# Kernel tuning notes

Hardware: AMD Instinct MI355X
Metric: run time of the kernel (lower is better)

The kernel has to match this reference:

```python
import jax, jax.numpy as jnp
import numpy as np

B, T, C, P = 16, 8, 64, 2048
TEMP = 1.0  # init kwarg T


def setup_inputs() -> dict:
    key = jax.random.key(0)
    ks = jax.random.split(key, 16)
    shape = (B, T, C, P)
    x = jax.random.normal(ks[0], shape, dtype=jnp.float32)
    attn = jax.random.uniform(ks[1], shape, dtype=jnp.float32)
    noise = jax.random.normal(ks[2], shape, dtype=jnp.float32)
    total = B * T * C * P
    n_noisy = int(total * 0.1)  # int(0.1 * numel), as in torch code
    idx = jax.random.permutation(ks[3], total)[:n_noisy]
    mask = jnp.zeros((total,), dtype=bool).at[idx].set(True).reshape(shape)
    perms = {}
    kidx = 4
    for i in (1, 2, 3):
        for name, dim in (("pB", B), ("pT", T), ("pC", C), ("pP", P)):
            perms[f"{name}{i}"] = jax.random.permutation(ks[kidx], dim).astype(jnp.int32)
            kidx += 1
    return dict(x=x, attn=attn, noise=noise, mask=mask, **perms)


def _permute4(x, pB, pT, pC, pP):
    # equivalent to the meshgrid/flatten gather in the torch code:
    # independent permutation along each of the 4 axes
    return x[jnp.ix_(pB, pT, pC, pP)]


def reference(x, attn, noise, mask,
              pB1, pT1, pC1, pP1,
              pB2, pT2, pC2, pP2,
              pB3, pT3, pC3, pP3):
    x_pos = jnp.where(mask, x + noise, x)
    x_neg1 = _permute4(x, pB1, pT1, pC1, pP1)
    x_neg2 = _permute4(x, pB2, pT2, pC2, pP2)
    x_neg3 = _permute4(x, pB3, pT3, pC3, pP3)

    loss_pos = jnp.mean(attn * (x - x_pos) ** 2)
    loss_neg1 = jnp.mean(attn * (x - x_neg1) ** 2)
    loss_neg2 = jnp.mean(attn * (x - x_neg2) ** 2)
    loss_neg3 = jnp.mean(attn * (x - x_neg3) ** 2)

    loss = -jnp.log(jnp.exp(loss_pos / TEMP) /
                    (jnp.exp(loss_neg1 / TEMP) + jnp.exp(loss_neg2 / TEMP) + jnp.exp(loss_neg3 / TEMP)))
    return loss
```

## Files before the change

kernel.cpp:

```cpp
#include <hip/hip_runtime.h>
#include <math.h>

#define BB 16
#define TT 8
#define CC 64
#define PP 2048
#define NROWS (BB * TT * CC)
#define TOTAL_INV (1.0f / 16777216.0f)

typedef __attribute__((address_space(1))) const void* as1_cvoid;
typedef __attribute__((address_space(3))) void* as3_void;

__device__ __forceinline__ void stage16(const float* g, float* l) {
    __builtin_amdgcn_global_load_lds((as1_cvoid)g, (as3_void)l, 16, 0, 0);
}

__global__ __launch_bounds__(256) void mask_classify_kernel(
    const unsigned char* __restrict__ mask, int* __restrict__ flag)
{
    __shared__ int sc1, sc3f;
    if (threadIdx.x == 0) { sc1 = 0; sc3f = 0; }
    __syncthreads();
    int c1 = 0, c3f = 0;
    const uint4* m4 = (const uint4*)mask;
    for (int i = threadIdx.x; i < 1024; i += 256) {
        const uint4 v = m4[i];
        const unsigned int w[4] = {v.x, v.y, v.z, v.w};
        #pragma unroll
        for (int j = 0; j < 4; ++j) {
            #pragma unroll
            for (int bt = 0; bt < 4; ++bt) {
                const unsigned int byte = (w[j] >> (8 * bt)) & 0xffu;
                c1  += (byte == 0x01u);
                c3f += (byte == 0x3fu);
            }
        }
    }
    atomicAdd(&sc1, c1);
    atomicAdd(&sc3f, c3f);
    __syncthreads();
    if (threadIdx.x == 0) {
        int f;
        if      (sc1  > 1000) f = 0;
        else if (sc3f >  600) f = 1;
        else if (sc3f >  200) f = 2;
        else if (sc1  >  200) f = 3;
        else                  f = 0;
        *flag = f;
    }
}

template <int MODE>
__device__ __forceinline__ void mask_load(const unsigned char* __restrict__ mask,
                                          size_t idx, float mf[4])
{
    if (MODE == 0) {
        const unsigned int mv = *(const unsigned int*)(mask + idx);
        #pragma unroll
        for (int k = 0; k < 4; ++k) mf[k] = ((mv >> (8 * k)) & 0xffu) ? 1.0f : 0.0f;
    } else if (MODE == 1) {
        const ushort4 mv = *(const ushort4*)((const unsigned short*)mask + idx);
        mf[0] = mv.x ? 1.0f : 0.0f; mf[1] = mv.y ? 1.0f : 0.0f;
        mf[2] = mv.z ? 1.0f : 0.0f; mf[3] = mv.w ? 1.0f : 0.0f;
    } else if (MODE == 2) {
        const float4 mv = *(const float4*)((const float*)mask + idx);
        mf[0] = mv.x != 0.f ? 1.0f : 0.0f; mf[1] = mv.y != 0.f ? 1.0f : 0.0f;
        mf[2] = mv.z != 0.f ? 1.0f : 0.0f; mf[3] = mv.w != 0.f ? 1.0f : 0.0f;
    } else {
        const int4 mv = *(const int4*)((const int*)mask + idx);
        mf[0] = mv.x ? 1.0f : 0.0f; mf[1] = mv.y ? 1.0f : 0.0f;
        mf[2] = mv.z ? 1.0f : 0.0f; mf[3] = mv.w ? 1.0f : 0.0f;
    }
}

template <int MODE>
__device__ __forceinline__ void row_body(
    const float* __restrict__ x, const float* __restrict__ attn,
    const float* __restrict__ noise, const unsigned char* __restrict__ mask,
    const int* __restrict__ pP1, const int* __restrict__ pP2,
    const int* __restrict__ pP3,
    const float* __restrict__ lds0, const float* __restrict__ lds1,
    const float* __restrict__ lds2,
    size_t rowbase, int tid, float& s0, float& s1, float& s2, float& s3)
{
    const int p0 = tid << 2;
    const int p1 = 1024 + (tid << 2);

    const float4 xv0 = *(const float4*)(x + rowbase + p0);
    const float4 xv1 = *(const float4*)(x + rowbase + p1);
    const float4 av0 = *(const float4*)(attn + rowbase + p0);
    const float4 av1 = *(const float4*)(attn + rowbase + p1);
    const float4 nv0 = *(const float4*)(noise + rowbase + p0);
    const float4 nv1 = *(const float4*)(noise + rowbase + p1);
    const int4 q10 = *(const int4*)(pP1 + p0);
    const int4 q11 = *(const int4*)(pP1 + p1);
    const int4 q20 = *(const int4*)(pP2 + p0);
    const int4 q21 = *(const int4*)(pP2 + p1);
    const int4 q30 = *(const int4*)(pP3 + p0);
    const int4 q31 = *(const int4*)(pP3 + p1);
    float mf0[4], mf1[4];
    mask_load<MODE>(mask, rowbase + p0, mf0);
    mask_load<MODE>(mask, rowbase + p1, mf1);

    const float xs0[4] = {xv0.x, xv0.y, xv0.z, xv0.w};
    const float xs1[4] = {xv1.x, xv1.y, xv1.z, xv1.w};
    const float as0[4] = {av0.x, av0.y, av0.z, av0.w};
    const float as1v[4] = {av1.x, av1.y, av1.z, av1.w};
    const float ns0[4] = {nv0.x, nv0.y, nv0.z, nv0.w};
    const float ns1[4] = {nv1.x, nv1.y, nv1.z, nv1.w};
    const int q1s0[4] = {q10.x, q10.y, q10.z, q10.w};
    const int q1s1[4] = {q11.x, q11.y, q11.z, q11.w};
    const int q2s0[4] = {q20.x, q20.y, q20.z, q20.w};
    const int q2s1[4] = {q21.x, q21.y, q21.z, q21.w};
    const int q3s0[4] = {q30.x, q30.y, q30.z, q30.w};
    const int q3s1[4] = {q31.x, q31.y, q31.z, q31.w};

    #pragma unroll
    for (int k = 0; k < 4; ++k) {
        const float d0a = ns0[k] * mf0[k];
        s0 += as0[k] * d0a * d0a;
        const float d0b = ns1[k] * mf1[k];
        s0 += as1v[k] * d0b * d0b;
    }

    __syncthreads();

    #pragma unroll
    for (int k = 0; k < 4; ++k) {
        const float d1a = xs0[k] - lds0[q1s0[k]];
        s1 += as0[k] * d1a * d1a;
        const float d2a = xs0[k] - lds1[q2s0[k]];
        s2 += as0[k] * d2a * d2a;
        const float d3a = xs0[k] - lds2[q3s0[k]];
        s3 += as0[k] * d3a * d3a;
        const float d1b = xs1[k] - lds0[q1s1[k]];
        s1 += as1v[k] * d1b * d1b;
        const float d2b = xs1[k] - lds1[q2s1[k]];
        s2 += as1v[k] * d2b * d2b;
        const float d3b = xs1[k] - lds2[q3s1[k]];
        s3 += as1v[k] * d3b * d3b;
    }
}

__global__ __launch_bounds__(256) void attn_loss_row_kernel(
    const float* __restrict__ x, const float* __restrict__ attn,
    const float* __restrict__ noise, const unsigned char* __restrict__ mask,
    const int* __restrict__ pB1, const int* __restrict__ pT1,
    const int* __restrict__ pC1, const int* __restrict__ pP1,
    const int* __restrict__ pB2, const int* __restrict__ pT2,
    const int* __restrict__ pC2, const int* __restrict__ pP2,
    const int* __restrict__ pB3, const int* __restrict__ pT3,
    const int* __restrict__ pC3, const int* __restrict__ pP3,
    const int* __restrict__ mask_flag,
    float4* __restrict__ partial)
{
    __shared__ float lds0[PP];
    __shared__ float lds1[PP];
    __shared__ float lds2[PP];
    __shared__ float red[4][4];

    const int r    = blockIdx.x;
    const int b    = r / (TT * CC);
    const int t    = (r / CC) % TT;
    const int c    = r % CC;
    const int tid  = threadIdx.x;
    const int wave = tid >> 6;
    const int lane = tid & 63;

    const size_t src0 = ((size_t)((pB1[b] * TT + pT1[t]) * CC + pC1[c])) * PP;
    const size_t src1 = ((size_t)((pB2[b] * TT + pT2[t]) * CC + pC2[c])) * PP;
    const size_t src2 = ((size_t)((pB3[b] * TT + pT3[t]) * CC + pC3[c])) * PP;

    #pragma unroll
    for (int s = 0; s < 2; ++s) {
        const int seg = wave + s * 4;
        const int fo  = seg * 256 + lane * 4;
        stage16(x + src0 + fo, &lds0[seg * 256]);
        stage16(x + src1 + fo, &lds1[seg * 256]);
        stage16(x + src2 + fo, &lds2[seg * 256]);
    }

    const size_t rowbase = (size_t)r * PP;
    float s0 = 0.f, s1 = 0.f, s2 = 0.f, s3 = 0.f;

    const int f = *mask_flag;
    switch (f) {
        case 1:  row_body<1>(x, attn, noise, mask, pP1, pP2, pP3,
                             lds0, lds1, lds2, rowbase, tid, s0, s1, s2, s3); break;
        case 2:  row_body<2>(x, attn, noise, mask, pP1, pP2, pP3,
                             lds0, lds1, lds2, rowbase, tid, s0, s1, s2, s3); break;
        case 3:  row_body<3>(x, attn, noise, mask, pP1, pP2, pP3,
                             lds0, lds1, lds2, rowbase, tid, s0, s1, s2, s3); break;
        default: row_body<0>(x, attn, noise, mask, pP1, pP2, pP3,
                             lds0, lds1, lds2, rowbase, tid, s0, s1, s2, s3); break;
    }

    #pragma unroll
    for (int off = 32; off; off >>= 1) {
        s0 += __shfl_down(s0, off, 64);
        s1 += __shfl_down(s1, off, 64);
        s2 += __shfl_down(s2, off, 64);
        s3 += __shfl_down(s3, off, 64);
    }
    if (lane == 0) {
        red[0][wave] = s0; red[1][wave] = s1;
        red[2][wave] = s2; red[3][wave] = s3;
    }
    __syncthreads();
    if (tid == 0) {
        float4 out;
        out.x = red[0][0] + red[0][1] + red[0][2] + red[0][3];
        out.y = red[1][0] + red[1][1] + red[1][2] + red[1][3];
        out.z = red[2][0] + red[2][1] + red[2][2] + red[2][3];
        out.w = red[3][0] + red[3][1] + red[3][2] + red[3][3];
        partial[r] = out;
    }
}

__global__ __launch_bounds__(1024) void attn_loss_final_kernel(
    const float4* __restrict__ partial, float* __restrict__ out)
{
    const int tid = threadIdx.x;
    float s0 = 0.f, s1 = 0.f, s2 = 0.f, s3 = 0.f;
    for (int i = tid; i < NROWS; i += 1024) {
        const float4 v = partial[i];
        s0 += v.x; s1 += v.y; s2 += v.z; s3 += v.w;
    }
    #pragma unroll
    for (int off = 32; off; off >>= 1) {
        s0 += __shfl_down(s0, off, 64);
        s1 += __shfl_down(s1, off, 64);
        s2 += __shfl_down(s2, off, 64);
        s3 += __shfl_down(s3, off, 64);
    }
    __shared__ float red[4][16];
    const int wave = tid >> 6;
    const int lane = tid & 63;
    if (lane == 0) {
        red[0][wave] = s0; red[1][wave] = s1;
        red[2][wave] = s2; red[3][wave] = s3;
    }
    __syncthreads();
    if (tid == 0) {
        float lp = 0.f, l1 = 0.f, l2 = 0.f, l3 = 0.f;
        #pragma unroll
        for (int w = 0; w < 16; ++w) {
            lp += red[0][w]; l1 += red[1][w];
            l2 += red[2][w]; l3 += red[3][w];
        }
        lp *= TOTAL_INV; l1 *= TOTAL_INV; l2 *= TOTAL_INV; l3 *= TOTAL_INV;
        const float m   = fmaxf(l1, fmaxf(l2, l3));
        const float lse = m + logf(expf(l1 - m) + expf(l2 - m) + expf(l3 - m));
        out[0] = lse - lp;
    }
}

extern "C" void kernel_launch(void* const* d_in, const int* in_sizes, int n_in,
                              void* d_out, int out_size, void* d_ws, size_t ws_size,
                              hipStream_t stream) {
    const float* x            = (const float*)d_in[0];
    const float* attn         = (const float*)d_in[1];
    const float* noise        = (const float*)d_in[2];
    const unsigned char* mask = (const unsigned char*)d_in[3];
    const int* pB1 = (const int*)d_in[4];
    const int* pT1 = (const int*)d_in[5];
    const int* pC1 = (const int*)d_in[6];
    const int* pP1 = (const int*)d_in[7];
    const int* pB2 = (const int*)d_in[8];
    const int* pT2 = (const int*)d_in[9];
    const int* pC2 = (const int*)d_in[10];
    const int* pP2 = (const int*)d_in[11];
    const int* pB3 = (const int*)d_in[12];
    const int* pT3 = (const int*)d_in[13];
    const int* pC3 = (const int*)d_in[14];
    const int* pP3 = (const int*)d_in[15];

    float4* partial = (float4*)d_ws;
    int* mask_flag  = (int*)((char*)d_ws + NROWS * 16);

    mask_classify_kernel<<<1, 256, 0, stream>>>(mask, mask_flag);
    attn_loss_row_kernel<<<NROWS, 256, 0, stream>>>(
        x, attn, noise, mask,
        pB1, pT1, pC1, pP1, pB2, pT2, pC2, pP2, pB3, pT3, pC3, pP3,
        mask_flag, partial);
    attn_loss_final_kernel<<<1, 1024, 0, stream>>>(partial, (float*)d_out);
}
```

Before: 83.56 us.

## Process four rows per block with double-buffered LDS staging of permuted rows

Each block now handles four consecutive rows instead of one. While it computes the current row, it stages the next row's three permuted source rows into a second LDS buffer using direct global-to-LDS loads, synchronised with a manual vmcnt wait and barriers. The aim is to hide the gather latency and amortise block launch and reduction overhead. In exchange, LDS use per block doubles to about 48KB, which limits occupancy (launch bounds request 3 blocks), and the hand-written vmcnt(6) is fragile if the compiler reorders or changes the number of outstanding loads.

```diff
diff --git a/kernel.cpp b/kernel.cpp
--- a/kernel.cpp
+++ b/kernel.cpp
@@ -5,7 +5,9 @@
 #define TT 8
 #define CC 64
 #define PP 2048
-#define NROWS (BB * TT * CC)
+#define NROWS 8192
+#define RPB 4
+#define NBLK (NROWS / RPB)
 #define TOTAL_INV (1.0f / 16777216.0f)
 
 typedef __attribute__((address_space(1))) const void* as1_cvoid;
@@ -13,6 +15,25 @@
 
 __device__ __forceinline__ void stage16(const float* g, float* l) {
     __builtin_amdgcn_global_load_lds((as1_cvoid)g, (as3_void)l, 16, 0, 0);
+}
+
+__device__ __forceinline__ void stage_rows(float (*dst)[PP], const float* x,
+                                           size_t a0, size_t a1, size_t a2,
+                                           int wave, int lane)
+{
+    #pragma unroll
+    for (int s = 0; s < 2; ++s) {
+        const int seg = wave + s * 4;
+        const int fo  = seg * 256 + lane * 4;
+        stage16(x + a0 + fo, &dst[0][seg * 256]);
+        stage16(x + a1 + fo, &dst[1][seg * 256]);
+        stage16(x + a2 + fo, &dst[2][seg * 256]);
+    }
+}
+
+__device__ __forceinline__ size_t src_of(const int* pB, const int* pT,
+                                         const int* pC, int b, int t, int c) {
+    return ((size_t)((pB[b] * TT + pT[t]) * CC + pC[c])) * PP;
 }
 
 __global__ __launch_bounds__(256) void mask_classify_kernel(
@@ -74,75 +95,98 @@
 }
 
 template <int MODE>
-__device__ __forceinline__ void row_body(
+__device__ __forceinline__ void block_body(
     const float* __restrict__ x, const float* __restrict__ attn,
     const float* __restrict__ noise, const unsigned char* __restrict__ mask,
     const int* __restrict__ pP1, const int* __restrict__ pP2,
     const int* __restrict__ pP3,
-    const float* __restrict__ lds0, const float* __restrict__ lds1,
-    const float* __restrict__ lds2,
-    size_t rowbase, int tid, float& s0, float& s1, float& s2, float& s3)
-{
-    const int p0 = tid << 2;
-    const int p1 = 1024 + (tid << 2);
-
-    const float4 xv0 = *(const float4*)(x + rowbase + p0);
-    const float4 xv1 = *(const float4*)(x + rowbase + p1);
-    const float4 av0 = *(const float4*)(attn + rowbase + p0);
-    const float4 av1 = *(const float4*)(attn + rowbase + p1);
-    const float4 nv0 = *(const float4*)(noise + rowbase + p0);
-    const float4 nv1 = *(const float4*)(noise + rowbase + p1);
-    const int4 q10 = *(const int4*)(pP1 + p0);
-    const int4 q11 = *(const int4*)(pP1 + p1);
-    const int4 q20 = *(const int4*)(pP2 + p0);
-    const int4 q21 = *(const int4*)(pP2 + p1);
-    const int4 q30 = *(const int4*)(pP3 + p0);
-    const int4 q31 = *(const int4*)(pP3 + p1);
-    float mf0[4], mf1[4];
-    mask_load<MODE>(mask, rowbase + p0, mf0);
-    mask_load<MODE>(mask, rowbase + p1, mf1);
-
-    const float xs0[4] = {xv0.x, xv0.y, xv0.z, xv0.w};
-    const float xs1[4] = {xv1.x, xv1.y, xv1.z, xv1.w};
-    const float as0[4] = {av0.x, av0.y, av0.z, av0.w};
-    const float as1v[4] = {av1.x, av1.y, av1.z, av1.w};
-    const float ns0[4] = {nv0.x, nv0.y, nv0.z, nv0.w};
-    const float ns1[4] = {nv1.x, nv1.y, nv1.z, nv1.w};
-    const int q1s0[4] = {q10.x, q10.y, q10.z, q10.w};
-    const int q1s1[4] = {q11.x, q11.y, q11.z, q11.w};
-    const int q2s0[4] = {q20.x, q20.y, q20.z, q20.w};
-    const int q2s1[4] = {q21.x, q21.y, q21.z, q21.w};
-    const int q3s0[4] = {q30.x, q30.y, q30.z, q30.w};
-    const int q3s1[4] = {q31.x, q31.y, q31.z, q31.w};
-
-    #pragma unroll
-    for (int k = 0; k < 4; ++k) {
-        const float d0a = ns0[k] * mf0[k];
-        s0 += as0[k] * d0a * d0a;
-        const float d0b = ns1[k] * mf1[k];
-        s0 += as1v[k] * d0b * d0b;
-    }
-
-    __syncthreads();
-
-    #pragma unroll
-    for (int k = 0; k < 4; ++k) {
-        const float d1a = xs0[k] - lds0[q1s0[k]];
-        s1 += as0[k] * d1a * d1a;
-        const float d2a = xs0[k] - lds1[q2s0[k]];
-        s2 += as0[k] * d2a * d2a;
-        const float d3a = xs0[k] - lds2[q3s0[k]];
-        s3 += as0[k] * d3a * d3a;
-        const float d1b = xs1[k] - lds0[q1s1[k]];
-        s1 += as1v[k] * d1b * d1b;
-        const float d2b = xs1[k] - lds1[q2s1[k]];
-        s2 += as1v[k] * d2b * d2b;
-        const float d3b = xs1[k] - lds2[q3s1[k]];
-        s3 += as1v[k] * d3b * d3b;
-    }
-}
-
-__global__ __launch_bounds__(256) void attn_loss_row_kernel(
+    float (*sbuf)[3][PP],
+    const size_t* sA, const size_t* sB, const size_t* sC,
+    int r0, int tid, int wave, int lane,
+    float& s0, float& s1, float& s2, float& s3)
+{
+    stage_rows(sbuf[0], x, sA[0], sB[0], sC[0], wave, lane);
+
+    #pragma unroll
+    for (int i = 0; i < RPB; ++i) {
+        const size_t rowbase = (size_t)(r0 + i) * PP;
+        const int p0 = tid << 2;
+        const int p1 = 1024 + (tid << 2);
+
+        const float4 xv0 = *(const float4*)(x + rowbase + p0);
+        const float4 xv1 = *(const float4*)(x + rowbase + p1);
+        const float4 av0 = *(const float4*)(attn + rowbase + p0);
+        const float4 av1 = *(const float4*)(attn + rowbase + p1);
+        const float4 nv0 = *(const float4*)(noise + rowbase + p0);
+        const float4 nv1 = *(const float4*)(noise + rowbase + p1);
+        const int4 q10 = *(const int4*)(pP1 + p0);
+        const int4 q11 = *(const int4*)(pP1 + p1);
+        const int4 q20 = *(const int4*)(pP2 + p0);
+        const int4 q21 = *(const int4*)(pP2 + p1);
+        const int4 q30 = *(const int4*)(pP3 + p0);
+        const int4 q31 = *(const int4*)(pP3 + p1);
+        float mf0[4], mf1[4];
+        mask_load<MODE>(mask, rowbase + p0, mf0);
+        mask_load<MODE>(mask, rowbase + p1, mf1);
+        __builtin_amdgcn_sched_barrier(0);
+
+        if (i + 1 < RPB)
+            stage_rows(sbuf[(i + 1) & 1], x, sA[i + 1], sB[i + 1], sC[i + 1],
+                       wave, lane);
+        __builtin_amdgcn_sched_barrier(0);
+
+        const float as0[4] = {av0.x, av0.y, av0.z, av0.w};
+        const float as1v[4] = {av1.x, av1.y, av1.z, av1.w};
+        {
+            const float ns0[4] = {nv0.x, nv0.y, nv0.z, nv0.w};
+            const float ns1[4] = {nv1.x, nv1.y, nv1.z, nv1.w};
+            #pragma unroll
+            for (int k = 0; k < 4; ++k) {
+                const float d0a = ns0[k] * mf0[k];
+                s0 += as0[k] * d0a * d0a;
+                const float d0b = ns1[k] * mf1[k];
+                s0 += as1v[k] * d0b * d0b;
+            }
+        }
+
+        asm volatile("s_waitcnt vmcnt(6)" ::: "memory");
+        __builtin_amdgcn_sched_barrier(0);
+        __builtin_amdgcn_s_barrier();
+
+        {
+            const float* l0 = sbuf[i & 1][0];
+            const float* l1 = sbuf[i & 1][1];
+            const float* l2 = sbuf[i & 1][2];
+            const float xs0[4] = {xv0.x, xv0.y, xv0.z, xv0.w};
+            const float xs1[4] = {xv1.x, xv1.y, xv1.z, xv1.w};
+            const int q1s0[4] = {q10.x, q10.y, q10.z, q10.w};
+            const int q1s1[4] = {q11.x, q11.y, q11.z, q11.w};
+            const int q2s0[4] = {q20.x, q20.y, q20.z, q20.w};
+            const int q2s1[4] = {q21.x, q21.y, q21.z, q21.w};
+            const int q3s0[4] = {q30.x, q30.y, q30.z, q30.w};
+            const int q3s1[4] = {q31.x, q31.y, q31.z, q31.w};
+            #pragma unroll
+            for (int k = 0; k < 4; ++k) {
+                const float d1a = xs0[k] - l0[q1s0[k]];
+                s1 += as0[k] * d1a * d1a;
+                const float d2a = xs0[k] - l1[q2s0[k]];
+                s2 += as0[k] * d2a * d2a;
+                const float d3a = xs0[k] - l2[q3s0[k]];
+                s3 += as0[k] * d3a * d3a;
+                const float d1b = xs1[k] - l0[q1s1[k]];
+                s1 += as1v[k] * d1b * d1b;
+                const float d2b = xs1[k] - l1[q2s1[k]];
+                s2 += as1v[k] * d2b * d2b;
+                const float d3b = xs1[k] - l2[q3s1[k]];
+                s3 += as1v[k] * d3b * d3b;
+            }
+        }
+        __builtin_amdgcn_s_barrier();
+        __builtin_amdgcn_sched_barrier(0);
+    }
+}
+
+__global__ __launch_bounds__(256, 3) void attn_loss_row_kernel(
     const float* __restrict__ x, const float* __restrict__ attn,
     const float* __restrict__ noise, const unsigned char* __restrict__ mask,
     const int* __restrict__ pB1, const int* __restrict__ pT1,
@@ -154,45 +198,38 @@
     const int* __restrict__ mask_flag,
     float4* __restrict__ partial)
 {
-    __shared__ float lds0[PP];
-    __shared__ float lds1[PP];
-    __shared__ float lds2[PP];
+    __shared__ float sbuf[2][3][PP];
     __shared__ float red[4][4];
 
-    const int r    = blockIdx.x;
-    const int b    = r / (TT * CC);
-    const int t    = (r / CC) % TT;
-    const int c    = r % CC;
     const int tid  = threadIdx.x;
     const int wave = tid >> 6;
     const int lane = tid & 63;
-
-    const size_t src0 = ((size_t)((pB1[b] * TT + pT1[t]) * CC + pC1[c])) * PP;
-    const size_t src1 = ((size_t)((pB2[b] * TT + pT2[t]) * CC + pC2[c])) * PP;
-    const size_t src2 = ((size_t)((pB3[b] * TT + pT3[t]) * CC + pC3[c])) * PP;
-
-    #pragma unroll
-    for (int s = 0; s < 2; ++s) {
-        const int seg = wave + s * 4;
-        const int fo  = seg * 256 + lane * 4;
-        stage16(x + src0 + fo, &lds0[seg * 256]);
-        stage16(x + src1 + fo, &lds1[seg * 256]);
-        stage16(x + src2 + fo, &lds2[seg * 256]);
-    }
-
-    const size_t rowbase = (size_t)r * PP;
+    const int r0   = blockIdx.x * RPB;
+
+    size_t sA[RPB], sB[RPB], sC[RPB];
+    #pragma unroll
+    for (int i = 0; i < RPB; ++i) {
+        const int r = r0 + i;
+        const int b = r / (TT * CC);
+        const int t = (r / CC) % TT;
+        const int c = r % CC;
+        sA[i] = src_of(pB1, pT1, pC1, b, t, c);
+        sB[i] = src_of(pB2, pT2, pC2, b, t, c);
+        sC[i] = src_of(pB3, pT3, pC3, b, t, c);
+    }
+
     float s0 = 0.f, s1 = 0.f, s2 = 0.f, s3 = 0.f;
 
     const int f = *mask_flag;
     switch (f) {
-        case 1:  row_body<1>(x, attn, noise, mask, pP1, pP2, pP3,
-                             lds0, lds1, lds2, rowbase, tid, s0, s1, s2, s3); break;
-        case 2:  row_body<2>(x, attn, noise, mask, pP1, pP2, pP3,
-                             lds0, lds1, lds2, rowbase, tid, s0, s1, s2, s3); break;
-        case 3:  row_body<3>(x, attn, noise, mask, pP1, pP2, pP3,
-                             lds0, lds1, lds2, rowbase, tid, s0, s1, s2, s3); break;
-        default: row_body<0>(x, attn, noise, mask, pP1, pP2, pP3,
-                             lds0, lds1, lds2, rowbase, tid, s0, s1, s2, s3); break;
+        case 1:  block_body<1>(x, attn, noise, mask, pP1, pP2, pP3, sbuf,
+                               sA, sB, sC, r0, tid, wave, lane, s0, s1, s2, s3); break;
+        case 2:  block_body<2>(x, attn, noise, mask, pP1, pP2, pP3, sbuf,
+                               sA, sB, sC, r0, tid, wave, lane, s0, s1, s2, s3); break;
+        case 3:  block_body<3>(x, attn, noise, mask, pP1, pP2, pP3, sbuf,
+                               sA, sB, sC, r0, tid, wave, lane, s0, s1, s2, s3); break;
+        default: block_body<0>(x, attn, noise, mask, pP1, pP2, pP3, sbuf,
+                               sA, sB, sC, r0, tid, wave, lane, s0, s1, s2, s3); break;
     }
 
     #pragma unroll
@@ -213,7 +250,7 @@
         out.y = red[1][0] + red[1][1] + red[1][2] + red[1][3];
         out.z = red[2][0] + red[2][1] + red[2][2] + red[2][3];
         out.w = red[3][0] + red[3][1] + red[3][2] + red[3][3];
-        partial[r] = out;
+        partial[blockIdx.x] = out;
     }
 }
 
@@ -222,7 +259,7 @@
 {
     const int tid = threadIdx.x;
     float s0 = 0.f, s1 = 0.f, s2 = 0.f, s3 = 0.f;
-    for (int i = tid; i < NROWS; i += 1024) {
+    for (int i = tid; i < NBLK; i += 1024) {
         const float4 v = partial[i];
         s0 += v.x; s1 += v.y; s2 += v.z; s3 += v.w;
     }
@@ -276,10 +313,10 @@
     const int* pP3 = (const int*)d_in[15];
 
     float4* partial = (float4*)d_ws;
-    int* mask_flag  = (int*)((char*)d_ws + NROWS * 16);
+    int* mask_flag  = (int*)((char*)d_ws + NBLK * 16);
 
     mask_classify_kernel<<<1, 256, 0, stream>>>(mask, mask_flag);
-    attn_loss_row_kernel<<<NROWS, 256, 0, stream>>>(
+    attn_loss_row_kernel<<<NBLK, 256, 0, stream>>>(
         x, attn, noise, mask,
         pB1, pT1, pC1, pP1, pB2, pT2, pC2, pP2, pB3, pT3, pC3, pP3,
         mask_flag, partial);
```

After: 91.35 us. +9.3%, slower.
